# Optimization experiments

Hardware: AMD Instinct MI355X
Metric: run time of the kernel (lower is better)

## Reference

```python
import jax, jax.numpy as jnp
import numpy as np

N_FFT = 512
HOP = 256
FS = 16000
D_INTER = 0.04
C_SOUND = 343.0
SOURCE_NUM = 2
EST_NUM = 4      # TF snapshots for the spatial covariance
T_START = 120    # starting frame of the snapshots
EPS = 1e-8
N_ANGLES = 361   # theta in [-90, 90] deg
T_SAMPLES = 3200000
N_MICS = 4


def _stft(xc):
    """xc: (C, T) real -> X: (C, F, n_frames) complex64.
    Matches torch.stft(center=True, pad_mode='reflect', onesided=True)
    with window = hann(N_FFT, periodic=True) ** 0.5.
    """
    n = jnp.arange(N_FFT, dtype=xc.dtype)
    win = jnp.sqrt(0.5 * (1.0 - jnp.cos(2.0 * jnp.pi * n / N_FFT)))  # hann^0.5
    pad = N_FFT // 2
    xp = jnp.pad(xc, ((0, 0), (pad, pad)), mode='reflect')
    n_frames = 1 + xc.shape[1] // HOP
    idx = jnp.arange(n_frames)[:, None] * HOP + jnp.arange(N_FFT)[None, :]
    frames = xp[:, idx] * win                     # (C, n_frames, N_FFT)
    X = jnp.fft.rfft(frames, axis=-1)             # (C, n_frames, F)
    return jnp.swapaxes(X, 1, 2)                  # (C, F, n_frames)


def setup_inputs() -> dict:
    key = jax.random.key(0)
    x = jax.random.normal(key, (T_SAMPLES, N_MICS), dtype=jnp.float32)
    return {"x": x}


def reference(x) -> jnp.ndarray:
    # ---- multi-channel STFT ----
    X = _stft(x.T)                                # (M, F, T_frames) complex64
    M = X.shape[0]

    # ---- spatial covariance from EST_NUM snapshots (vectorized over bins) ----
    Xs = X[:, :, T_START:T_START + EST_NUM]       # (M, F, EST_NUM)
    spt = jnp.einsum('mft,nft->fmn', Xs, jnp.conj(Xs)) / EST_NUM  # (F, M, M) Hermitian

    # ---- noise subspace via Hermitian eigendecomposition ----
    # eigh returns ascending eigenvalues; take the M-SOURCE_NUM smallest
    # (noise) eigenvectors, i.e. descending order then columns SOURCE_NUM:.
    _, V = jnp.linalg.eigh(spt)                   # (F, M, M)
    noise = V[:, :, ::-1][:, :, SOURCE_NUM:]      # (F, M, M-SOURCE_NUM)

    # ---- spatial spectrum, fully batched over all 361 angles ----
    f_analog = jnp.linspace(0.0, FS / 2, N_FFT // 2 + 1, dtype=jnp.float32)
    theta = jnp.deg2rad(jnp.linspace(-90.0, 90.0, N_ANGLES, dtype=jnp.float32))
    mics = jnp.arange(M, dtype=jnp.float32)
    # phase: (A, F, M)
    phase = (2.0 * jnp.pi * D_INTER / C_SOUND) * (
        jnp.sin(theta)[:, None, None] * f_analog[None, :, None] * mics[None, None, :]
    )
    steer = jnp.exp(-1j * phase).astype(jnp.complex64)            # (A, F, M)
    mid = jnp.einsum('afm,fmk->afk', steer, noise)                # (A, F, K)
    val = jnp.sum(mid.real ** 2 + mid.imag ** 2, axis=-1)         # (A, F)
    spt_spec = jnp.mean(1.0 / (val + EPS), axis=1)                # (A,)
    return spt_spec
```

## Files before the change

### kernel.cpp

```cpp
#include <hip/hip_runtime.h>
#include <math.h>

#define NFFT   512
#define HOP    256
#define NFREQ  257
#define NMIC   4
#define TSTART 120
#define NANG   361

static constexpr double PI_D = 3.14159265358979323846;
static constexpr float  PI_F = 3.14159265358979323846f;

__global__ __launch_bounds__(512)
void stft_kernel(const float* __restrict__ x,
                 float* __restrict__ part_re,
                 float* __restrict__ part_im) {
    int b = blockIdx.x;
    int chunk = b >> 4;
    int m = (b >> 2) & 3;
    int t = b & 3;
    int tid = threadIdx.x;

    __shared__ float2 tw[512];
    __shared__ float  v[128];

    {
        float ang = (2.0f * PI_F / 512.0f) * (float)tid;
        float s, c;
        sincosf(ang, &s, &c);
        tw[tid] = make_float2(c, s);
    }
    if (tid < 128) {
        int n = chunk * 128 + tid;
        long base = ((long)(TSTART + t - 1) * HOP) * NMIC + m;
        v[tid] = x[base + (long)n * NMIC] * sinf(PI_F * (float)n / 512.0f);
    }
    __syncthreads();

    int f = tid;
    if (f >= NFREQ) return;
    int k = (f * (chunk * 128)) & 511;
    float re = 0.0f, im = 0.0f;
#pragma unroll 4
    for (int j = 0; j < 128; ++j) {
        float vn = v[j];
        float2 cs = tw[k];
        re += vn * cs.x;
        im -= vn * cs.y;
        k = (k + f) & 511;
    }
    int id = f * 16 + m * 4 + t;
    part_re[chunk * 4112 + id] = re;
    part_im[chunk * 4112 + id] = im;
}

__global__ __launch_bounds__(64)
void eig_kernel(const float* __restrict__ part_re,
                const float* __restrict__ part_im,
                float* __restrict__ coef) {
    int f = blockIdx.x * blockDim.x + threadIdx.x;
    if (f >= NFREQ) return;

    float Xr[4][4], Xi[4][4];
#pragma unroll
    for (int m = 0; m < 4; ++m)
#pragma unroll
        for (int t = 0; t < 4; ++t) {
            int id = f * 16 + m * 4 + t;
            Xr[m][t] = part_re[id] + part_re[4112 + id]
                     + part_re[2 * 4112 + id] + part_re[3 * 4112 + id];
            Xi[m][t] = part_im[id] + part_im[4112 + id]
                     + part_im[2 * 4112 + id] + part_im[3 * 4112 + id];
        }

    float Ar[4][4], Ai[4][4];
#pragma unroll
    for (int m = 0; m < 4; ++m)
#pragma unroll
        for (int n = 0; n < 4; ++n) {
            float rr = 0.0f, ii = 0.0f;
#pragma unroll
            for (int t = 0; t < 4; ++t) {
                rr += Xr[m][t] * Xr[n][t] + Xi[m][t] * Xi[n][t];
                ii += Xi[m][t] * Xr[n][t] - Xr[m][t] * Xi[n][t];
            }
            Ar[m][n] = rr;
            Ai[m][n] = ii;
        }

    float Vr[4][4] = {{1,0,0,0},{0,1,0,0},{0,0,1,0},{0,0,0,1}};
    float Vi[4][4] = {{0,0,0,0},{0,0,0,0},{0,0,0,0},{0,0,0,0}};

    for (int sweep = 0; sweep < 6; ++sweep) {
#pragma unroll
        for (int p = 0; p < 3; ++p)
#pragma unroll
            for (int q = p + 1; q < 4; ++q) {
                float ar = Ar[p][q], ai = Ai[p][q];
                float n2 = ar * ar + ai * ai;
                bool ok = n2 > 1e-24f;
                float n2s = ok ? n2 : 1.0f;
                float inv = 1.0f / sqrtf(n2s);
                float er = ar * inv, ei = ai * inv;
                float tau = (Ar[q][q] - Ar[p][p]) * (0.5f * inv * (ok ? 1.0f : 0.0f));
                float t_ = (tau >= 0.0f ? 1.0f : -1.0f) /
                           (fabsf(tau) + sqrtf(1.0f + tau * tau));
                float c = ok ? 1.0f / sqrtf(1.0f + t_ * t_) : 1.0f;
                float s = ok ? t_ * c : 0.0f;
#pragma unroll
                for (int k = 0; k < 4; ++k) {
                    float apr = Ar[k][p], api = Ai[k][p];
                    float aqr = Ar[k][q], aqi = Ai[k][q];
                    float tr = er * aqr + ei * aqi;
                    float ti = er * aqi - ei * aqr;
                    Ar[k][p] = c * apr - s * tr;
                    Ai[k][p] = c * api - s * ti;
                    float ur = er * apr - ei * api;
                    float ui = er * api + ei * apr;
                    Ar[k][q] = s * ur + c * aqr;
                    Ai[k][q] = s * ui + c * aqi;
                }
#pragma unroll
                for (int k = 0; k < 4; ++k) {
                    float apr = Ar[p][k], api = Ai[p][k];
                    float aqr = Ar[q][k], aqi = Ai[q][k];
                    float tr = er * aqr - ei * aqi;
                    float ti = er * aqi + ei * aqr;
                    Ar[p][k] = c * apr - s * tr;
                    Ai[p][k] = c * api - s * ti;
                    float ur = er * apr + ei * api;
                    float ui = er * api - ei * apr;
                    Ar[q][k] = s * ur + c * aqr;
                    Ai[q][k] = s * ui + c * aqi;
                }
#pragma unroll
                for (int k = 0; k < 4; ++k) {
                    float apr = Vr[k][p], api = Vi[k][p];
                    float aqr = Vr[k][q], aqi = Vi[k][q];
                    float tr = er * aqr + ei * aqi;
                    float ti = er * aqi - ei * aqr;
                    Vr[k][p] = c * apr - s * tr;
                    Vi[k][p] = c * api - s * ti;
                    float ur = er * apr - ei * api;
                    float ui = er * api + ei * apr;
                    Vr[k][q] = s * ur + c * aqr;
                    Vi[k][q] = s * ui + c * aqi;
                }
            }
    }

    float dd[4] = {Ar[0][0], Ar[1][1], Ar[2][2], Ar[3][3]};
    float w[4];
#pragma unroll
    for (int j = 0; j < 4; ++j) {
        int rank = 0;
#pragma unroll
        for (int k = 0; k < 4; ++k) {
            if (k == j) continue;
            bool less = (dd[k] < dd[j]) || (dd[k] == dd[j] && k < j);
            rank += less ? 1 : 0;
        }
        w[j] = (rank < 2) ? 1.0f : 0.0f;
    }

    float s1r = 0.f, s1i = 0.f, s2r = 0.f, s2i = 0.f, s3r = 0.f, s3i = 0.f, trc = 0.f;
#pragma unroll
    for (int j = 0; j < 4; ++j) {
        float wj = w[j];
        s1r += wj * (Vr[0][j]*Vr[1][j] + Vi[0][j]*Vi[1][j]
                   + Vr[1][j]*Vr[2][j] + Vi[1][j]*Vi[2][j]
                   + Vr[2][j]*Vr[3][j] + Vi[2][j]*Vi[3][j]);
        s1i += wj * (Vi[0][j]*Vr[1][j] - Vr[0][j]*Vi[1][j]
                   + Vi[1][j]*Vr[2][j] - Vr[1][j]*Vi[2][j]
                   + Vi[2][j]*Vr[3][j] - Vr[2][j]*Vi[3][j]);
        s2r += wj * (Vr[0][j]*Vr[2][j] + Vi[0][j]*Vi[2][j]
                   + Vr[1][j]*Vr[3][j] + Vi[1][j]*Vi[3][j]);
        s2i += wj * (Vi[0][j]*Vr[2][j] - Vr[0][j]*Vi[2][j]
                   + Vi[1][j]*Vr[3][j] - Vr[1][j]*Vi[3][j]);
        s3r += wj * (Vr[0][j]*Vr[3][j] + Vi[0][j]*Vi[3][j]);
        s3i += wj * (Vi[0][j]*Vr[3][j] - Vr[0][j]*Vi[3][j]);
        trc += wj * (Vr[0][j]*Vr[0][j] + Vi[0][j]*Vi[0][j]
                   + Vr[1][j]*Vr[1][j] + Vi[1][j]*Vi[1][j]
                   + Vr[2][j]*Vr[2][j] + Vi[2][j]*Vi[2][j]
                   + Vr[3][j]*Vr[3][j] + Vi[3][j]*Vi[3][j]);
    }
    float* cf = coef + f * 8;
    cf[0] = s1r; cf[1] = s1i; cf[2] = s2r; cf[3] = s2i;
    cf[4] = s3r; cf[5] = s3i; cf[6] = trc; cf[7] = 0.0f;
}

__global__ __launch_bounds__(320)
void music_kernel(const float* __restrict__ coef,
                  float* __restrict__ out) {
    int a = blockIdx.x;
    int tid = threadIdx.x;
    float r = 0.0f;
    if (tid < NFREQ) {
        const float4* cf4 = (const float4*)(coef + tid * 8);
        float4 cA = cf4[0];
        float4 cB = cf4[1];
        float theta = (-90.0f + 0.5f * (float)a) * (PI_F / 180.0f);
        float freq = 31.25f * (float)tid;
        float phi = (float)(2.0 * PI_D * 0.04 / 343.0) * sinf(theta) * freq;
        float s1, c1;
        sincosf(phi, &s1, &c1);
        float c2 = c1 * c1 - s1 * s1;
        float s2 = 2.0f * s1 * c1;
        float c3 = c1 * c2 - s1 * s2;
        float s3 = s1 * c2 + c1 * s2;
        float val = cB.z + 2.0f * (c1 * cA.x - s1 * cA.y
                                 + c2 * cA.z - s2 * cA.w
                                 + c3 * cB.x - s3 * cB.y);
        r = 1.0f / (val + 1e-8f);
    }
#pragma unroll
    for (int off = 32; off > 0; off >>= 1)
        r += __shfl_down(r, off, 64);
    __shared__ float ps[5];
    if ((tid & 63) == 0) ps[tid >> 6] = r;
    __syncthreads();
    if (tid == 0)
        out[a] = (ps[0] + ps[1] + ps[2] + ps[3] + ps[4]) / 257.0f;
}

extern "C" void kernel_launch(void* const* d_in, const int* in_sizes, int n_in,
                              void* d_out, int out_size, void* d_ws, size_t ws_size,
                              hipStream_t stream) {
    const float* x = (const float*)d_in[0];
    float* out = (float*)d_out;

    float* part_re = (float*)d_ws;
    float* part_im = part_re + 4 * 4112;
    float* coef    = part_im + 4 * 4112;

    stft_kernel<<<64, 512, 0, stream>>>(x, part_re, part_im);
    eig_kernel<<<(NFREQ + 63) / 64, 64, 0, stream>>>(part_re, part_im, coef);
    music_kernel<<<NANG, 320, 0, stream>>>(coef, out);
}
```

Measured before the change: 108.5 us.

## Replace twiddle table with rotation recurrence, cut Jacobi sweeps, use fast rsq/rcp

The STFT kernel no longer builds a shared-memory twiddle table. Each thread now computes its starting phase with sincosf and advances it by complex-rotation multiplies, removing the per-iteration LDS gather and one barrier dependency. The eigen kernel runs 4 Jacobi sweeps instead of 6 and uses hardware rsq/rcp intrinsics in place of IEEE divide and sqrt. These changes cut latency on small serial kernels but accumulate rotation error over 128 steps, and the fewer sweeps may leave the 4x4 eigendecomposition less converged.

```diff
diff --git a/kernel.cpp b/kernel.cpp
--- a/kernel.cpp
+++ b/kernel.cpp
@@ -21,15 +21,8 @@
     int t = b & 3;
     int tid = threadIdx.x;
 
-    __shared__ float2 tw[512];
-    __shared__ float  v[128];
-
-    {
-        float ang = (2.0f * PI_F / 512.0f) * (float)tid;
-        float s, c;
-        sincosf(ang, &s, &c);
-        tw[tid] = make_float2(c, s);
-    }
+    __shared__ float v[128];
+
     if (tid < 128) {
         int n = chunk * 128 + tid;
         long base = ((long)(TSTART + t - 1) * HOP) * NMIC + m;
@@ -39,22 +32,30 @@
 
     int f = tid;
     if (f >= NFREQ) return;
-    int k = (f * (chunk * 128)) & 511;
+
+    float c, s, cd, sd;
+    {
+        int k0 = (f * (chunk * 128)) & 511;
+        int kd = f & 511;
+        sincosf(-2.0f * PI_F * (float)k0 / 512.0f, &s, &c);
+        sincosf(-2.0f * PI_F * (float)kd / 512.0f, &sd, &cd);
+    }
     float re = 0.0f, im = 0.0f;
 #pragma unroll 4
     for (int j = 0; j < 128; ++j) {
         float vn = v[j];
-        float2 cs = tw[k];
-        re += vn * cs.x;
-        im -= vn * cs.y;
-        k = (k + f) & 511;
+        re += vn * c;
+        im += vn * s;
+        float cn = c * cd - s * sd;
+        s = s * cd + c * sd;
+        c = cn;
     }
     int id = f * 16 + m * 4 + t;
     part_re[chunk * 4112 + id] = re;
     part_im[chunk * 4112 + id] = im;
 }
 
-__global__ __launch_bounds__(64)
+__global__ __launch_bounds__(64, 1)
 void eig_kernel(const float* __restrict__ part_re,
                 const float* __restrict__ part_im,
                 float* __restrict__ coef) {
@@ -91,7 +92,7 @@
     float Vr[4][4] = {{1,0,0,0},{0,1,0,0},{0,0,1,0},{0,0,0,1}};
     float Vi[4][4] = {{0,0,0,0},{0,0,0,0},{0,0,0,0},{0,0,0,0}};
 
-    for (int sweep = 0; sweep < 6; ++sweep) {
+    for (int sweep = 0; sweep < 4; ++sweep) {
 #pragma unroll
         for (int p = 0; p < 3; ++p)
 #pragma unroll
@@ -100,12 +101,12 @@
                 float n2 = ar * ar + ai * ai;
                 bool ok = n2 > 1e-24f;
                 float n2s = ok ? n2 : 1.0f;
-                float inv = 1.0f / sqrtf(n2s);
+                float inv = __builtin_amdgcn_rsqf(n2s);
                 float er = ar * inv, ei = ai * inv;
                 float tau = (Ar[q][q] - Ar[p][p]) * (0.5f * inv * (ok ? 1.0f : 0.0f));
-                float t_ = (tau >= 0.0f ? 1.0f : -1.0f) /
-                           (fabsf(tau) + sqrtf(1.0f + tau * tau));
-                float c = ok ? 1.0f / sqrtf(1.0f + t_ * t_) : 1.0f;
+                float t_ = (tau >= 0.0f ? 1.0f : -1.0f) *
+                           __builtin_amdgcn_rcpf(fabsf(tau) + sqrtf(1.0f + tau * tau));
+                float c = ok ? __builtin_amdgcn_rsqf(1.0f + t_ * t_) : 1.0f;
                 float s = ok ? t_ * c : 0.0f;
 #pragma unroll
                 for (int k = 0; k < 4; ++k) {
```

New measurement: 101.4 us. -6.5%, faster.
